# Kernel optimization log

Hardware: AMD Instinct MI355X
Metric: run time of the kernel (lower is better)

Reference implementation:

```python
import jax, jax.numpy as jnp
import numpy as np

L = 10   # lattice side (hardcoded self.length)
K = 3    # kernel_size -> half_k = 1 wrap padding
FN = 4   # filter_num
B = 262144


def setup_inputs() -> dict:
    key = jax.random.key(0)
    k1, k2, k3, k4, k5 = jax.random.split(key, 5)
    v = jax.random.normal(k1, (B, L * L), dtype=jnp.float32)
    # torch default init scale ~ 1/sqrt(fan_in)
    conv_w = jax.random.normal(k2, (FN, 1, K, K), dtype=jnp.float32) / 3.0
    conv_b = jax.random.normal(k3, (FN,), dtype=jnp.float32) * 0.1
    deconv_w = jax.random.normal(k4, (FN, 1, 2, 2), dtype=jnp.float32) / 4.0
    deconv_b = jax.random.normal(k5, (1,), dtype=jnp.float32) * 0.1
    data = jnp.zeros((1,), dtype=jnp.int32)  # unused positional arg of log_psi
    return {"v": v, "conv_w": conv_w, "conv_b": conv_b,
            "deconv_w": deconv_w, "deconv_b": deconv_b, "data": data}


def _log_psi(v, conv_w, conv_b, deconv_w, deconv_b):
    b = v.shape[0]
    x = v.reshape(b, 1, L, L)
    # handmade_padding == periodic (wrap) pad of width half_k=1 on both spatial axes
    x = jnp.pad(x, ((0, 0), (0, 0), (1, 1), (1, 1)), mode="wrap")  # [B,1,12,12]
    # Conv2d(1, FN, 3), VALID -> [B,FN,10,10]
    y = jax.lax.conv_general_dilated(
        x, conv_w, window_strides=(1, 1), padding="VALID",
        dimension_numbers=("NCHW", "OIHW", "NCHW"))
    y = y + conv_b[None, :, None, None]
    # MaxPool2d(2,2): non-overlapping 2x2 -> [B,FN,5,5]
    y = y.reshape(b, FN, L // 2, 2, L // 2, 2).max(axis=(3, 5))
    # ConvTranspose2d(FN,1,kernel=2,stride=2): each input pixel -> disjoint 2x2 block
    # torch weight layout [in=FN, out=1, 2, 2]
    z = jnp.einsum("bcij,cokl->boikjl", y, deconv_w).reshape(b, 1, L, L)
    z = z + deconv_b[None, :, None, None]
    sign_z = jnp.sign(z)
    abs_z = z * sign_z
    sign_prod = sign_z.reshape(b, -1).prod(axis=1)        # scalar per sample
    log_sum = jnp.log(abs_z).reshape(b, -1).sum(axis=1)   # scalar per sample
    return sign_prod, log_sum


def reference(v, conv_w, conv_b, deconv_w, deconv_b, data):
    return _log_psi(v, conv_w, conv_b, deconv_w, deconv_b)
```

## Files before the change

### kernel.cpp

```cpp
#include <hip/hip_runtime.h>
#include <math.h>


typedef float v2f __attribute__((ext_vector_type(2)));

#define SREAD(x) __int_as_float(__builtin_amdgcn_readfirstlane(__float_as_int(x)))
#define WAITVM(N) asm volatile("s_waitcnt vmcnt(" #N ")" ::: "memory")
#define MEMFENCE() asm volatile("" ::: "memory")

__device__ __forceinline__ float dpp_swap1_f(float x) {
    return __int_as_float(__builtin_amdgcn_mov_dpp(__float_as_int(x), 0xB1, 0xF, 0xF, true));
}
__device__ __forceinline__ float dpp_swap2_f(float x) {
    return __int_as_float(__builtin_amdgcn_mov_dpp(__float_as_int(x), 0x4E, 0xF, 0xF, true));
}
__device__ __forceinline__ unsigned dpp_swap1_u(unsigned x) {
    return (unsigned)__builtin_amdgcn_mov_dpp((int)x, 0xB1, 0xF, 0xF, true);
}
__device__ __forceinline__ unsigned dpp_swap2_u(unsigned x) {
    return (unsigned)__builtin_amdgcn_mov_dpp((int)x, 0x4E, 0xF, 0xF, true);
}

__device__ __forceinline__ void gload16(const float* g, float* l) {
    __builtin_amdgcn_global_load_lds(
        (const __attribute__((address_space(1))) void*)g,
        (__attribute__((address_space(3))) void*)l, 16, 0, 0);
}
__device__ __forceinline__ void gload4(const float* g, float* l) {
    __builtin_amdgcn_global_load_lds(
        (const __attribute__((address_space(1))) void*)g,
        (__attribute__((address_space(3))) void*)l, 4, 0, 0);
}

__global__ __launch_bounds__(64, 4) void CNN2D_37495064494620_kernel(
    const float* __restrict__ v,
    const float* __restrict__ cw,
    const float* __restrict__ cb,
    const float* __restrict__ dw,
    const float* __restrict__ db,
    float* __restrict__ out,
    int B)
{
    const int lane = threadIdx.x;
    const int q    = lane & 1;
    const int h    = (lane >> 1) & 1;
    const int g    = lane >> 2;

    __shared__ __align__(16) float sm[3200];

    float Wf[4][9];
    #pragma unroll
    for (int f = 0; f < 4; ++f)
        #pragma unroll
        for (int t = 0; t < 9; ++t)
            Wf[f][t] = SREAD(cw[f * 9 + t]);
    v2f Wsel[9];
    #pragma unroll
    for (int t = 0; t < 9; ++t)
        Wsel[t] = (v2f){ h ? Wf[2][t] : Wf[0][t], h ? Wf[3][t] : Wf[1][t] };
    const float cb0 = SREAD(cb[0]), cb1 = SREAD(cb[1]);
    const float cb2 = SREAD(cb[2]), cb3 = SREAD(cb[3]);
    const v2f Cbsel = (v2f){ h ? cb2 : cb0, h ? cb3 : cb1 };

    float Dw4[4][4];
    #pragma unroll
    for (int f = 0; f < 4; ++f)
        #pragma unroll
        for (int t = 0; t < 4; ++t)
            Dw4[f][t] = SREAD(dw[f * 4 + t]);
    const float Db = SREAD(db[0]);
    float Dkl[4];
    #pragma unroll
    for (int f = 0; f < 4; ++f) {
        const float e01 = h ? Dw4[f][1] : Dw4[f][0];
        const float e23 = h ? Dw4[f][3] : Dw4[f][2];
        Dkl[f] = q ? e23 : e01;
    }
    const float Ds0 = h ? Dkl[2] : Dkl[0];
    const float Ds1 = h ? Dkl[3] : Dkl[1];
    const float Ds2 = h ? Dkl[0] : Dkl[2];
    const float Ds3 = h ? Dkl[1] : Dkl[3];

    WAITVM(0);

    const float* gbase = v + (size_t)blockIdx.x * 3200;

    auto STAGE = [&](int b) {
        const float* gb = gbase + b * 1600;
        float* lb = sm + b * 1600;
        #pragma unroll
        for (int k = 0; k < 6; ++k)
            gload16(gb + k * 256 + lane * 4, lb + k * 256);
        gload4(gb + 1536 + lane, lb + 1536);
    };

    auto COMPUTE = [&](const float* buf, int sbase) {
        const float* my = buf + g * 100;
        unsigned sb = 0u;
        float l2 = 0.0f;
        float zpend = 0.0f;

        #pragma unroll
        for (int i = 0; i < 5; ++i) {
            const int r1 = 2 * i + q;
            const int r0 = (i == 0) ? (q ? 0 : 9) : (2 * i - 1 + q);
            const int r2 = (i == 4) ? (q ? 0 : 9) : (2 * i + 1 + q);

            float R[3][10];
            #pragma unroll
            for (int t = 0; t < 5; ++t) {
                float2 x0 = *(const float2*)(my + r0 * 10 + 2 * t);
                float2 x1 = *(const float2*)(my + r1 * 10 + 2 * t);
                float2 x2 = *(const float2*)(my + r2 * 10 + 2 * t);
                R[0][2 * t] = x0.x; R[0][2 * t + 1] = x0.y;
                R[1][2 * t] = x1.x; R[1][2 * t + 1] = x1.y;
                R[2][2 * t] = x2.x; R[2][2 * t + 1] = x2.y;
            }

            #pragma unroll
            for (int j = 0; j < 5; ++j) {
                v2f a0 = Cbsel, a1 = Cbsel;
                #pragma unroll
                for (int kr = 0; kr < 3; ++kr) {
                    #pragma unroll
                    for (int kc = 0; kc < 3; ++kc) {
                        const int cc0 = (2 * j + kc + 9) % 10;
                        const int cc1 = (2 * j + 1 + kc + 9) % 10;
                        const int t = kr * 3 + kc;
                        const v2f x0 = (v2f){R[kr][cc0], R[kr][cc0]};
                        const v2f x1 = (v2f){R[kr][cc1], R[kr][cc1]};
                        a0 = __builtin_elementwise_fma(x0, Wsel[t], a0);
                        a1 = __builtin_elementwise_fma(x1, Wsel[t], a1);
                    }
                }
                const v2f m = __builtin_elementwise_max(a0, a1);
                const float Px = fmaxf(m.x, dpp_swap1_f(m.x));
                const float Py = fmaxf(m.y, dpp_swap1_f(m.y));
                const float Qx = dpp_swap2_f(Px);
                const float Qy = dpp_swap2_f(Py);
                float z = Db;
                z = fmaf(Px, Ds0, z);
                z = fmaf(Py, Ds1, z);
                z = fmaf(Qx, Ds2, z);
                z = fmaf(Qy, Ds3, z);

                const int pos = i * 5 + j;
                if (pos == 24) {
                    sb ^= __float_as_uint(z);
                    l2 += __log2f(fabsf(z));
                } else if (pos & 1) {
                    const float zp = zpend * z;
                    sb ^= __float_as_uint(zp);
                    l2 += __log2f(fabsf(zp));
                } else {
                    zpend = z;
                }
            }
        }

        l2 += dpp_swap1_f(l2);
        l2 += dpp_swap2_f(l2);
        sb ^= dpp_swap1_u(sb);
        sb ^= dpp_swap2_u(sb);

        const int s = sbase + g;
        const int r = lane & 3;
        if (r == 0)      out[s]     = (sb & 0x80000000u) ? -1.0f : 1.0f;
        else if (r == 1) out[B + s] = l2 * 0.69314718055994531f;
    };

    STAGE(0);
    MEMFENCE();
    STAGE(1);

    const int sb0 = blockIdx.x * 32;
    WAITVM(7);
    COMPUTE(sm, sb0);
    WAITVM(0);
    COMPUTE(sm + 1600, sb0 + 16);
}

extern "C" void kernel_launch(void* const* d_in, const int* in_sizes, int n_in,
                              void* d_out, int out_size, void* d_ws, size_t ws_size,
                              hipStream_t stream) {
    const float* v  = (const float*)d_in[0];
    const float* cw = (const float*)d_in[1];
    const float* cb = (const float*)d_in[2];
    const float* dw = (const float*)d_in[3];
    const float* db = (const float*)d_in[4];
    float* out = (float*)d_out;

    const int B = in_sizes[0] / 100;
    const int grid = B / 32;
    CNN2D_37495064494620_kernel<<<grid, 64, 0, stream>>>(v, cw, cb, dw, db, out, B);
}
```

Measured before the change: 169.4 us.

## Split sample batches across two waves and reuse shared input rows

Each 128-thread block now runs two wavefronts, and each wave owns one 16-sample tile in LDS. This replaces the old single wave that staged two tiles and processed them one after the other. The global-to-LDS loads are issued before the weight setup so they overlap with it. The conv row loads are restructured so the shared boundary row between consecutive pooled rows is kept in registers and reused, which cuts LDS reads from 3 rows to about 2 per step. The change loses the explicit two-stage overlap within a wave and relies on more resident waves to hide load latency. Launch bounds change to 128 threads with 6 blocks per CU.

```diff
diff --git a/kernel.cpp b/kernel.cpp
--- a/kernel.cpp
+++ b/kernel.cpp
@@ -6,7 +6,6 @@
 
 #define SREAD(x) __int_as_float(__builtin_amdgcn_readfirstlane(__float_as_int(x)))
 #define WAITVM(N) asm volatile("s_waitcnt vmcnt(" #N ")" ::: "memory")
-#define MEMFENCE() asm volatile("" ::: "memory")
 
 __device__ __forceinline__ float dpp_swap1_f(float x) {
     return __int_as_float(__builtin_amdgcn_mov_dpp(__float_as_int(x), 0xB1, 0xF, 0xF, true));
@@ -32,7 +31,7 @@
         (__attribute__((address_space(3))) void*)l, 4, 0, 0);
 }
 
-__global__ __launch_bounds__(64, 4) void CNN2D_37495064494620_kernel(
+__global__ __launch_bounds__(128, 6) void CNN2D_37495064494620_kernel(
     const float* __restrict__ v,
     const float* __restrict__ cw,
     const float* __restrict__ cb,
@@ -41,12 +40,20 @@
     float* __restrict__ out,
     int B)
 {
-    const int lane = threadIdx.x;
+    const int lane = threadIdx.x & 63;
+    const int w    = threadIdx.x >> 6;
     const int q    = lane & 1;
     const int h    = (lane >> 1) & 1;
     const int g    = lane >> 2;
 
-    __shared__ __align__(16) float sm[3200];
+    __shared__ __align__(16) float smraw[3200];
+    float* sm = smraw + w * 1600;
+
+    const float* gb = v + (size_t)(blockIdx.x * 2 + w) * 1600;
+    #pragma unroll
+    for (int k = 0; k < 6; ++k)
+        gload16(gb + k * 256 + lane * 4, sm + k * 256);
+    gload4(gb + 1536 + lane, sm + 1536);
 
     float Wf[4][9];
     #pragma unroll
@@ -83,101 +90,94 @@
 
     WAITVM(0);
 
-    const float* gbase = v + (size_t)blockIdx.x * 3200;
+    const float* my  = sm + g * 100;
+    const float* myq = my + q * 10;
+    const float* mx  = my + (q ? 0 : 90);
 
-    auto STAGE = [&](int b) {
-        const float* gb = gbase + b * 1600;
-        float* lb = sm + b * 1600;
+    auto load5 = [&](float* dst, const float* src) {
         #pragma unroll
-        for (int k = 0; k < 6; ++k)
-            gload16(gb + k * 256 + lane * 4, lb + k * 256);
-        gload4(gb + 1536 + lane, lb + 1536);
+        for (int t = 0; t < 5; ++t) {
+            float2 x = *(const float2*)(src + 2 * t);
+            dst[2 * t] = x.x; dst[2 * t + 1] = x.y;
+        }
     };
 
-    auto COMPUTE = [&](const float* buf, int sbase) {
-        const float* my = buf + g * 100;
-        unsigned sb = 0u;
-        float l2 = 0.0f;
-        float zpend = 0.0f;
+    unsigned sb = 0u;
+    float l2 = 0.0f;
+    float zpend = 0.0f;
+
+    float X[2][10];
+    float RB[10];
+    load5(X[0], mx);
+
+    #pragma unroll
+    for (int i = 0; i < 5; ++i) {
+        load5(RB, myq + 20 * i);
+        load5(X[(i + 1) & 1], (i == 4) ? mx : (myq + 10 + 20 * i));
+        const float* R0 = X[i & 1];
+        const float* R1 = RB;
+        const float* R2 = X[(i + 1) & 1];
 
         #pragma unroll
-        for (int i = 0; i < 5; ++i) {
-            const int r1 = 2 * i + q;
-            const int r0 = (i == 0) ? (q ? 0 : 9) : (2 * i - 1 + q);
-            const int r2 = (i == 4) ? (q ? 0 : 9) : (2 * i + 1 + q);
-
-            float R[3][10];
+        for (int j = 0; j < 5; ++j) {
+            v2f a0 = Cbsel, a1 = Cbsel;
             #pragma unroll
-            for (int t = 0; t < 5; ++t) {
-                float2 x0 = *(const float2*)(my + r0 * 10 + 2 * t);
-                float2 x1 = *(const float2*)(my + r1 * 10 + 2 * t);
-                float2 x2 = *(const float2*)(my + r2 * 10 + 2 * t);
-                R[0][2 * t] = x0.x; R[0][2 * t + 1] = x0.y;
-                R[1][2 * t] = x1.x; R[1][2 * t + 1] = x1.y;
-                R[2][2 * t] = x2.x; R[2][2 * t + 1] = x2.y;
-            }
-
-            #pragma unroll
-            for (int j = 0; j < 5; ++j) {
-                v2f a0 = Cbsel, a1 = Cbsel;
-                #pragma unroll
-                for (int kr = 0; kr < 3; ++kr) {
-                    #pragma unroll
-                    for (int kc = 0; kc < 3; ++kc) {
-                        const int cc0 = (2 * j + kc + 9) % 10;
-                        const int cc1 = (2 * j + 1 + kc + 9) % 10;
-                        const int t = kr * 3 + kc;
-                        const v2f x0 = (v2f){R[kr][cc0], R[kr][cc0]};
-                        const v2f x1 = (v2f){R[kr][cc1], R[kr][cc1]};
-                        a0 = __builtin_elementwise_fma(x0, Wsel[t], a0);
-                        a1 = __builtin_elementwise_fma(x1, Wsel[t], a1);
-                    }
+            for (int kc = 0; kc < 3; ++kc) {
+                const int cc0 = (2 * j + kc + 9) % 10;
+                const int cc1 = (2 * j + 1 + kc + 9) % 10;
+                {
+                    const v2f x0 = (v2f){R0[cc0], R0[cc0]};
+                    const v2f x1 = (v2f){R0[cc1], R0[cc1]};
+                    a0 = __builtin_elementwise_fma(x0, Wsel[kc], a0);
+                    a1 = __builtin_elementwise_fma(x1, Wsel[kc], a1);
                 }
-                const v2f m = __builtin_elementwise_max(a0, a1);
-                const float Px = fmaxf(m.x, dpp_swap1_f(m.x));
-                const float Py = fmaxf(m.y, dpp_swap1_f(m.y));
-                const float Qx = dpp_swap2_f(Px);
-                const float Qy = dpp_swap2_f(Py);
-                float z = Db;
-                z = fmaf(Px, Ds0, z);
-                z = fmaf(Py, Ds1, z);
-                z = fmaf(Qx, Ds2, z);
-                z = fmaf(Qy, Ds3, z);
-
-                const int pos = i * 5 + j;
-                if (pos == 24) {
-                    sb ^= __float_as_uint(z);
-                    l2 += __log2f(fabsf(z));
-                } else if (pos & 1) {
-                    const float zp = zpend * z;
-                    sb ^= __float_as_uint(zp);
-                    l2 += __log2f(fabsf(zp));
-                } else {
-                    zpend = z;
+                {
+                    const v2f x0 = (v2f){R1[cc0], R1[cc0]};
+                    const v2f x1 = (v2f){R1[cc1], R1[cc1]};
+                    a0 = __builtin_elementwise_fma(x0, Wsel[3 + kc], a0);
+                    a1 = __builtin_elementwise_fma(x1, Wsel[3 + kc], a1);
+                }
+                {
+                    const v2f x0 = (v2f){R2[cc0], R2[cc0]};
+                    const v2f x1 = (v2f){R2[cc1], R2[cc1]};
+                    a0 = __builtin_elementwise_fma(x0, Wsel[6 + kc], a0);
+                    a1 = __builtin_elementwise_fma(x1, Wsel[6 + kc], a1);
                 }
             }
+            const v2f m = __builtin_elementwise_max(a0, a1);
+            const float Px = fmaxf(m.x, dpp_swap1_f(m.x));
+            const float Py = fmaxf(m.y, dpp_swap1_f(m.y));
+            const float Qx = dpp_swap2_f(Px);
+            const float Qy = dpp_swap2_f(Py);
+            float z = Db;
+            z = fmaf(Px, Ds0, z);
+            z = fmaf(Py, Ds1, z);
+            z = fmaf(Qx, Ds2, z);
+            z = fmaf(Qy, Ds3, z);
+
+            const int pos = i * 5 + j;
+            if (pos == 24) {
+                sb ^= __float_as_uint(z);
+                l2 += __log2f(fabsf(z));
+            } else if (pos & 1) {
+                const float zp = zpend * z;
+                sb ^= __float_as_uint(zp);
+                l2 += __log2f(fabsf(zp));
+            } else {
+                zpend = z;
+            }
         }
+    }
 
-        l2 += dpp_swap1_f(l2);
-        l2 += dpp_swap2_f(l2);
-        sb ^= dpp_swap1_u(sb);
-        sb ^= dpp_swap2_u(sb);
+    l2 += dpp_swap1_f(l2);
+    l2 += dpp_swap2_f(l2);
+    sb ^= dpp_swap1_u(sb);
+    sb ^= dpp_swap2_u(sb);
 
-        const int s = sbase + g;
-        const int r = lane & 3;
-        if (r == 0)      out[s]     = (sb & 0x80000000u) ? -1.0f : 1.0f;
-        else if (r == 1) out[B + s] = l2 * 0.69314718055994531f;
-    };
-
-    STAGE(0);
-    MEMFENCE();
-    STAGE(1);
-
-    const int sb0 = blockIdx.x * 32;
-    WAITVM(7);
-    COMPUTE(sm, sb0);
-    WAITVM(0);
-    COMPUTE(sm + 1600, sb0 + 16);
+    const int s = blockIdx.x * 32 + w * 16 + g;
+    const int r = lane & 3;
+    if (r == 0)      out[s]     = (sb & 0x80000000u) ? -1.0f : 1.0f;
+    else if (r == 1) out[B + s] = l2 * 0.69314718055994531f;
 }
 
 extern "C" void kernel_launch(void* const* d_in, const int* in_sizes, int n_in,
@@ -192,5 +192,5 @@
 
     const int B = in_sizes[0] / 100;
     const int grid = B / 32;
-    CNN2D_37495064494620_kernel<<<grid, 64, 0, stream>>>(v, cw, cb, dw, db, out, B);
+    CNN2D_37495064494620_kernel<<<grid, 128, 0, stream>>>(v, cw, cb, dw, db, out, B);
 }
```

Measured after the change: 186.5 us. 1.1x slower.

## Interleave both sample halves in one compute pass and issue all loads up front

Applied to the files above, without the earlier changes.

Issues both halves of the block's global-to-LDS loads before the weight broadcast and waits for all of them at once, dropping the staged wait that let compute on the first half overlap the second half's load. The two 16-sample computations are interleaved in one loop so the independent FMA chains and DPP shuffles can hide each other's latency. Output stores are spread across four lanes instead of two. Removing the occupancy hint from the launch bounds and holding two register tiles raises register pressure, which may lower occupancy or cause spills.

```diff
diff --git a/kernel.cpp b/kernel.cpp
--- a/kernel.cpp
+++ b/kernel.cpp
@@ -6,7 +6,6 @@
 
 #define SREAD(x) __int_as_float(__builtin_amdgcn_readfirstlane(__float_as_int(x)))
 #define WAITVM(N) asm volatile("s_waitcnt vmcnt(" #N ")" ::: "memory")
-#define MEMFENCE() asm volatile("" ::: "memory")
 
 __device__ __forceinline__ float dpp_swap1_f(float x) {
     return __int_as_float(__builtin_amdgcn_mov_dpp(__float_as_int(x), 0xB1, 0xF, 0xF, true));
@@ -32,7 +31,7 @@
         (__attribute__((address_space(3))) void*)l, 4, 0, 0);
 }
 
-__global__ __launch_bounds__(64, 4) void CNN2D_37495064494620_kernel(
+__global__ __launch_bounds__(64) void CNN2D_37495064494620_kernel(
     const float* __restrict__ v,
     const float* __restrict__ cw,
     const float* __restrict__ cb,
@@ -48,6 +47,16 @@
 
     __shared__ __align__(16) float sm[3200];
 
+    const float* gb = v + (size_t)blockIdx.x * 3200;
+    #pragma unroll
+    for (int k = 0; k < 6; ++k)
+        gload16(gb + k * 256 + lane * 4, sm + k * 256);
+    gload4(gb + 1536 + lane, sm + 1536);
+    #pragma unroll
+    for (int k = 0; k < 6; ++k)
+        gload16(gb + 1600 + k * 256 + lane * 4, sm + 1600 + k * 256);
+    gload4(gb + 3136 + lane, sm + 3136);
+
     float Wf[4][9];
     #pragma unroll
     for (int f = 0; f < 4; ++f)
@@ -83,101 +92,107 @@
 
     WAITVM(0);
 
-    const float* gbase = v + (size_t)blockIdx.x * 3200;
-
-    auto STAGE = [&](int b) {
-        const float* gb = gbase + b * 1600;
-        float* lb = sm + b * 1600;
-        #pragma unroll
-        for (int k = 0; k < 6; ++k)
-            gload16(gb + k * 256 + lane * 4, lb + k * 256);
-        gload4(gb + 1536 + lane, lb + 1536);
-    };
-
-    auto COMPUTE = [&](const float* buf, int sbase) {
-        const float* my = buf + g * 100;
-        unsigned sb = 0u;
-        float l2 = 0.0f;
-        float zpend = 0.0f;
-
-        #pragma unroll
-        for (int i = 0; i < 5; ++i) {
-            const int r1 = 2 * i + q;
-            const int r0 = (i == 0) ? (q ? 0 : 9) : (2 * i - 1 + q);
-            const int r2 = (i == 4) ? (q ? 0 : 9) : (2 * i + 1 + q);
-
-            float R[3][10];
+    const float* myA = sm + g * 100;
+    const float* myB = sm + 1600 + g * 100;
+
+    unsigned sbA = 0u, sbB = 0u;
+    float l2A = 0.0f, l2B = 0.0f;
+    float zpA = 0.0f, zpB = 0.0f;
+
+    #pragma unroll
+    for (int i = 0; i < 5; ++i) {
+        const int r1 = 2 * i + q;
+        const int r0 = (i == 0) ? (q ? 0 : 9) : (2 * i - 1 + q);
+        const int r2 = (i == 4) ? (q ? 0 : 9) : (2 * i + 1 + q);
+
+        float RA[3][10], RB[3][10];
+        #pragma unroll
+        for (int t = 0; t < 5; ++t) {
+            float2 a0v = *(const float2*)(myA + r0 * 10 + 2 * t);
+            float2 a1v = *(const float2*)(myA + r1 * 10 + 2 * t);
+            float2 a2v = *(const float2*)(myA + r2 * 10 + 2 * t);
+            RA[0][2 * t] = a0v.x; RA[0][2 * t + 1] = a0v.y;
+            RA[1][2 * t] = a1v.x; RA[1][2 * t + 1] = a1v.y;
+            RA[2][2 * t] = a2v.x; RA[2][2 * t + 1] = a2v.y;
+            float2 b0v = *(const float2*)(myB + r0 * 10 + 2 * t);
+            float2 b1v = *(const float2*)(myB + r1 * 10 + 2 * t);
+            float2 b2v = *(const float2*)(myB + r2 * 10 + 2 * t);
+            RB[0][2 * t] = b0v.x; RB[0][2 * t + 1] = b0v.y;
+            RB[1][2 * t] = b1v.x; RB[1][2 * t + 1] = b1v.y;
+            RB[2][2 * t] = b2v.x; RB[2][2 * t + 1] = b2v.y;
+        }
+
+        #pragma unroll
+        for (int j = 0; j < 5; ++j) {
+            const int pos = i * 5 + j;
+
+            v2f a0A = Cbsel, a1A = Cbsel, a0B = Cbsel, a1B = Cbsel;
             #pragma unroll
-            for (int t = 0; t < 5; ++t) {
-                float2 x0 = *(const float2*)(my + r0 * 10 + 2 * t);
-                float2 x1 = *(const float2*)(my + r1 * 10 + 2 * t);
-                float2 x2 = *(const float2*)(my + r2 * 10 + 2 * t);
-                R[0][2 * t] = x0.x; R[0][2 * t + 1] = x0.y;
-                R[1][2 * t] = x1.x; R[1][2 * t + 1] = x1.y;
-                R[2][2 * t] = x2.x; R[2][2 * t + 1] = x2.y;
-            }
-
-            #pragma unroll
-            for (int j = 0; j < 5; ++j) {
-                v2f a0 = Cbsel, a1 = Cbsel;
+            for (int kr = 0; kr < 3; ++kr) {
                 #pragma unroll
-                for (int kr = 0; kr < 3; ++kr) {
-                    #pragma unroll
-                    for (int kc = 0; kc < 3; ++kc) {
-                        const int cc0 = (2 * j + kc + 9) % 10;
-                        const int cc1 = (2 * j + 1 + kc + 9) % 10;
-                        const int t = kr * 3 + kc;
-                        const v2f x0 = (v2f){R[kr][cc0], R[kr][cc0]};
-                        const v2f x1 = (v2f){R[kr][cc1], R[kr][cc1]};
-                        a0 = __builtin_elementwise_fma(x0, Wsel[t], a0);
-                        a1 = __builtin_elementwise_fma(x1, Wsel[t], a1);
-                    }
-                }
-                const v2f m = __builtin_elementwise_max(a0, a1);
-                const float Px = fmaxf(m.x, dpp_swap1_f(m.x));
-                const float Py = fmaxf(m.y, dpp_swap1_f(m.y));
-                const float Qx = dpp_swap2_f(Px);
-                const float Qy = dpp_swap2_f(Py);
-                float z = Db;
-                z = fmaf(Px, Ds0, z);
-                z = fmaf(Py, Ds1, z);
-                z = fmaf(Qx, Ds2, z);
-                z = fmaf(Qy, Ds3, z);
-
-                const int pos = i * 5 + j;
-                if (pos == 24) {
-                    sb ^= __float_as_uint(z);
-                    l2 += __log2f(fabsf(z));
-                } else if (pos & 1) {
-                    const float zp = zpend * z;
-                    sb ^= __float_as_uint(zp);
-                    l2 += __log2f(fabsf(zp));
-                } else {
-                    zpend = z;
+                for (int kc = 0; kc < 3; ++kc) {
+                    const int cc0 = (2 * j + kc + 9) % 10;
+                    const int cc1 = (2 * j + 1 + kc + 9) % 10;
+                    const int t = kr * 3 + kc;
+                    const v2f xA0 = (v2f){RA[kr][cc0], RA[kr][cc0]};
+                    const v2f xA1 = (v2f){RA[kr][cc1], RA[kr][cc1]};
+                    a0A = __builtin_elementwise_fma(xA0, Wsel[t], a0A);
+                    a1A = __builtin_elementwise_fma(xA1, Wsel[t], a1A);
+                    const v2f xB0 = (v2f){RB[kr][cc0], RB[kr][cc0]};
+                    const v2f xB1 = (v2f){RB[kr][cc1], RB[kr][cc1]};
+                    a0B = __builtin_elementwise_fma(xB0, Wsel[t], a0B);
+                    a1B = __builtin_elementwise_fma(xB1, Wsel[t], a1B);
                 }
             }
+
+            const v2f mA = __builtin_elementwise_max(a0A, a1A);
+            const v2f mB = __builtin_elementwise_max(a0B, a1B);
+            const float PxA = fmaxf(mA.x, dpp_swap1_f(mA.x));
+            const float PxB = fmaxf(mB.x, dpp_swap1_f(mB.x));
+            const float PyA = fmaxf(mA.y, dpp_swap1_f(mA.y));
+            const float PyB = fmaxf(mB.y, dpp_swap1_f(mB.y));
+            const float QxA = dpp_swap2_f(PxA);
+            const float QxB = dpp_swap2_f(PxB);
+            const float QyA = dpp_swap2_f(PyA);
+            const float QyB = dpp_swap2_f(PyB);
+
+            float zA = Db, zB = Db;
+            zA = fmaf(PxA, Ds0, zA);  zB = fmaf(PxB, Ds0, zB);
+            zA = fmaf(PyA, Ds1, zA);  zB = fmaf(PyB, Ds1, zB);
+            zA = fmaf(QxA, Ds2, zA);  zB = fmaf(QxB, Ds2, zB);
+            zA = fmaf(QyA, Ds3, zA);  zB = fmaf(QyB, Ds3, zB);
+
+            if (pos == 24) {
+                sbA ^= __float_as_uint(zA);
+                l2A += __log2f(fabsf(zA));
+                sbB ^= __float_as_uint(zB);
+                l2B += __log2f(fabsf(zB));
+            } else if (pos & 1) {
+                const float zpa = zpA * zA;
+                const float zpb = zpB * zB;
+                sbA ^= __float_as_uint(zpa);
+                sbB ^= __float_as_uint(zpb);
+                l2A += __log2f(fabsf(zpa));
+                l2B += __log2f(fabsf(zpb));
+            } else {
+                zpA = zA;
+                zpB = zB;
+            }
         }
-
-        l2 += dpp_swap1_f(l2);
-        l2 += dpp_swap2_f(l2);
-        sb ^= dpp_swap1_u(sb);
-        sb ^= dpp_swap2_u(sb);
-
-        const int s = sbase + g;
-        const int r = lane & 3;
-        if (r == 0)      out[s]     = (sb & 0x80000000u) ? -1.0f : 1.0f;
-        else if (r == 1) out[B + s] = l2 * 0.69314718055994531f;
-    };
-
-    STAGE(0);
-    MEMFENCE();
-    STAGE(1);
-
-    const int sb0 = blockIdx.x * 32;
-    WAITVM(7);
-    COMPUTE(sm, sb0);
-    WAITVM(0);
-    COMPUTE(sm + 1600, sb0 + 16);
+    }
+
+    l2A += dpp_swap1_f(l2A);  l2B += dpp_swap1_f(l2B);
+    l2A += dpp_swap2_f(l2A);  l2B += dpp_swap2_f(l2B);
+    sbA ^= dpp_swap1_u(sbA);  sbB ^= dpp_swap1_u(sbB);
+    sbA ^= dpp_swap2_u(sbA);  sbB ^= dpp_swap2_u(sbB);
+
+    const int sA = blockIdx.x * 32 + g;
+    const int sB = sA + 16;
+    const int r = lane & 3;
+    if (r == 0)      out[sA]     = (sbA & 0x80000000u) ? -1.0f : 1.0f;
+    else if (r == 1) out[B + sA] = l2A * 0.69314718055994531f;
+    else if (r == 2) out[sB]     = (sbB & 0x80000000u) ? -1.0f : 1.0f;
+    else             out[B + sB] = l2B * 0.69314718055994531f;
 }
 
 extern "C" void kernel_launch(void* const* d_in, const int* in_sizes, int n_in,
```

Measured after the change: 168.1 us. Within noise of the previous version (-0.8%).
